# Performance work log

Measured on AMD Instinct MI355X. Metric: run time of the kernel, lower is better.

Reference implementation:

```python
import jax, jax.numpy as jnp
import numpy as np

DN = ('NCHW', 'OIHW', 'NCHW')

def _conv(x, w, padding):
    return jax.lax.conv_general_dilated(
        x, w, window_strides=(1, 1), padding=padding,
        dimension_numbers=DN)

def setup_inputs() -> dict:
    key = jax.random.key(0)
    k1, k2, k3, k4, k5 = jax.random.split(key, 5)
    nf = 40
    x = jax.random.normal(k1, (16, nf, 256, 256), dtype=jnp.float32)
    # PyTorch conv default init scale ~ 1/sqrt(fan_in)
    w2 = jax.random.normal(k2, (nf, nf, 1, 1), dtype=jnp.float32) / np.sqrt(nf)
    b2 = jax.random.normal(k3, (nf,), dtype=jnp.float32) * 0.01
    w3 = jax.random.normal(k4, (nf, nf, 3, 3), dtype=jnp.float32) / np.sqrt(nf * 9)
    w4 = jax.random.normal(k5, (nf, nf, 3, 3), dtype=jnp.float32) / np.sqrt(nf * 9)
    return {"x": x, "w2": w2, "b2": b2, "w3": w3, "w4": w4}

def reference(x, w2, b2, w3, w4):
    # k2: 1x1 conv + bias, then sigmoid gate (pixel attention)
    y = _conv(x, w2, padding='VALID') + b2[None, :, None, None]
    y = jax.nn.sigmoid(y)
    # k3: 3x3 conv (pad 1, no bias), gated elementwise
    out = _conv(x, w3, padding=((1, 1), (1, 1))) * y
    # k4: 3x3 conv (pad 1, no bias)
    out = _conv(out, w4, padding=((1, 1), (1, 1)))
    return out
```

## Files before the change

kernel.cpp:

```cpp
#include <hip/hip_runtime.h>
#include <hip/hip_bf16.h>

typedef __bf16 bf16;
typedef __bf16 bf16x2 __attribute__((ext_vector_type(2)));
typedef __bf16 bf16x4 __attribute__((ext_vector_type(4)));
typedef __bf16 bf16x8 __attribute__((ext_vector_type(8)));
typedef float f32x4 __attribute__((ext_vector_type(4)));

#define NF 40
#define HW 256
#define KPAD 384
#define MPAD 48

#define ZROW_ELEM_OFF (2 * MPAD * KPAD + MPAD * 64)
#define GATED_ELEM_OFF 40960
#define IMG_ELEMS ((size_t)16 * HW * HW * NF)
#define XT_ELEM_OFF (GATED_ELEM_OFF + IMG_ELEMS)
#define WS_FULL  ((GATED_ELEM_OFF + 2 * IMG_ELEMS) * 2)

#define PLANE ((size_t)HW * HW * 8)
#define IMGSTR ((size_t)HW * HW * NF)

#define RW 34
#define RU 612
#define GS 4896
#define NUNITS 3060
#define XS_ELEMS 24576

__device__ __forceinline__ void gload_lds16(const bf16* g, bf16* l) {
  __builtin_amdgcn_global_load_lds(
      (const __attribute__((address_space(1))) void*)g,
      (__attribute__((address_space(3))) void*)l, 16, 0, 0);
}

__global__ void prep_weights(const float* __restrict__ w2,
                             const float* __restrict__ w3,
                             const float* __restrict__ w4,
                             bf16* __restrict__ ws) {
  int i = blockIdx.x * 256 + threadIdx.x;
  const int T = MPAD * KPAD;
  if (i < T) {
    int co = i / KPAD, k = i % KPAD;
    float v3 = 0.f, v4 = 0.f;
    if (co < NF && k < 360) {
      int tap = k / NF, ci = k - tap * NF;
      int ky = tap / 3, kx = tap - ky * 3;
      int idx = ((co * NF + ci) * 3 + ky) * 3 + kx;
      v3 = w3[idx];
      v4 = w4[idx];
    }
    ws[i] = (bf16)v3;
    ws[T + i] = (bf16)v4;
  }
  if (i < MPAD * 64) {
    int co = i / 64, ci = i - co * 64;
    float v = 0.f;
    if (co < NF && ci < NF) v = w2[co * NF + ci];
    ws[2 * T + i] = (bf16)v;
  }
  if (i < 1024) ws[ZROW_ELEM_OFF + i] = (bf16)0.f;
}

__global__ __launch_bounds__(256, 8)
void transpose_nhwc(const float* __restrict__ x, bf16* __restrict__ xT) {
  __shared__ bf16 xs[5 * 2056];
  const int tid = threadIdx.x;
  const int row = blockIdx.x;
  const int n   = blockIdx.y;
  const size_t nb = (size_t)n * NF * HW * HW + (size_t)row * HW;

#pragma unroll
  for (int cc = 0; cc < 10; ++cc) {
    bf16x4 v;
#pragma unroll
    for (int j = 0; j < 4; ++j)
      v[j] = (bf16)x[nb + (size_t)(cc * 4 + j) * HW * HW + tid];
    *(bf16x4*)&xs[(cc >> 1) * 2056 + tid * 8 + (cc & 1) * 4] = v;
  }
  __syncthreads();

  const size_t ob = ((size_t)n * HW * HW + (size_t)row * HW) * NF;
#pragma unroll
  for (int k = 0; k < 10; ++k) {
    int u = tid + k * 256;
    int px = u / 10, c4 = u - px * 10;
    bf16x4 v = *(const bf16x4*)&xs[(c4 >> 1) * 2056 + px * 8 + (c4 & 1) * 4];
    *(bf16x4*)&xT[ob + (size_t)u * 4] = v;
  }
}

__global__ __launch_bounds__(512, 4)
void k1_gate(const bf16* __restrict__ xT, const float* __restrict__ b2,
             const bf16* __restrict__ ws, bf16* __restrict__ gated) {
  __shared__ bf16 xs[XS_ELEMS];

  const int tid  = threadIdx.x;
  const int lane = tid & 63;
  const int wid  = tid >> 6;
  const int l15  = lane & 15;
  const int lk   = lane >> 4;
  const int n    = blockIdx.z;
  const int X0   = blockIdx.x * 32;
  const int Y0   = blockIdx.y * 16;

  const bf16* W3A  = ws;
  const bf16* W2A  = ws + 2 * MPAD * KPAD;
  const bf16* zrow = ws + ZROW_ELEM_OFF;

  const bf16* bn = xT + (size_t)n * IMGSTR;
#pragma unroll
  for (int it = 0; it < 6; ++it) {
    int u0 = it * 512 + wid * 64;
    int u  = u0 + lane;
    int c   = u / RU;
    int rem = u - c * RU;
    int r   = rem / RW;
    int p   = rem - r * RW;
    int gy  = Y0 - 1 + r, gx = X0 - 1 + p;
    bool ok = (u < NUNITS) && ((unsigned)gy < HW) && ((unsigned)gx < HW);
    const bf16* src = ok ? (bn + (size_t)(gy * HW + gx) * NF + (c << 3)) : zrow;
    gload_lds16(src, &xs[u0 * 8]);
  }

  int gp3[12];
#pragma unroll
  for (int kk = 0; kk < 12; ++kk) {
    int k0 = kk * 32 + lk * 8;
    int kc = (k0 < 360) ? k0 : 0;
    int tap = kc / NF, ci0 = kc - tap * NF;
    int ky = tap / 3, kx = tap - ky * 3;
    gp3[kk] = (ci0 >> 3) * GS + (ky * RW + kx) * 8;
  }
  int gctr[2];
#pragma unroll
  for (int kk = 0; kk < 2; ++kk) {
    int k0 = kk * 32 + lk * 8;
    int ci0 = (k0 < NF) ? k0 : 0;
    gctr[kk] = (ci0 >> 3) * GS + (RW + 1) * 8;
  }
  int pb[4];
#pragma unroll
  for (int g = 0; g < 4; ++g) {
    int prow = wid * 2 + (g >> 1);
    int pcol = (g & 1) * 16 + l15;
    pb[g] = (prow * RW + pcol) * 8;
  }
  float b2v[3][4];
#pragma unroll
  for (int mt = 0; mt < 3; ++mt)
#pragma unroll
    for (int r = 0; r < 4; ++r) {
      int co = mt * 16 + lk * 4 + r;
      b2v[mt][r] = (co < NF) ? b2[co] : 0.f;
    }
  bf16x8 a2[2][3];
#pragma unroll
  for (int kk = 0; kk < 2; ++kk)
#pragma unroll
    for (int mt = 0; mt < 3; ++mt)
      a2[kk][mt] = *(const bf16x8*)&W2A[(mt * 16 + l15) * 64 + kk * 32 + lk * 8];

  __syncthreads();

  bf16x4 gv[4][3];
  {
    f32x4 g[4][3];
#pragma unroll
    for (int q = 0; q < 4; ++q)
#pragma unroll
      for (int mt = 0; mt < 3; ++mt) g[q][mt] = f32x4{0, 0, 0, 0};
#pragma unroll
    for (int kk = 0; kk < 2; ++kk)
#pragma unroll
      for (int q = 0; q < 4; ++q) {
        bf16x8 b = *(const bf16x8*)&xs[gctr[kk] + pb[q]];
#pragma unroll
        for (int mt = 0; mt < 3; ++mt)
          g[q][mt] = __builtin_amdgcn_mfma_f32_16x16x32_bf16(a2[kk][mt], b, g[q][mt], 0, 0, 0);
      }
#pragma unroll
    for (int q = 0; q < 4; ++q)
#pragma unroll
      for (int mt = 0; mt < 3; ++mt)
#pragma unroll
        for (int r = 0; r < 4; ++r)
          gv[q][mt][r] = (bf16)(1.f / (1.f + __expf(-(g[q][mt][r] + b2v[mt][r]))));
  }

  f32x4 f[4][3];
#pragma unroll
  for (int q = 0; q < 4; ++q)
#pragma unroll
    for (int mt = 0; mt < 3; ++mt) f[q][mt] = f32x4{0, 0, 0, 0};

#pragma unroll
  for (int kk = 0; kk < 12; ++kk) {
    bf16x8 a[3];
#pragma unroll
    for (int mt = 0; mt < 3; ++mt)
      a[mt] = *(const bf16x8*)&W3A[(mt * 16 + l15) * KPAD + kk * 32 + lk * 8];
#pragma unroll
    for (int q = 0; q < 4; ++q) {
      bf16x8 b = *(const bf16x8*)&xs[gp3[kk] + pb[q]];
#pragma unroll
      for (int mt = 0; mt < 3; ++mt)
        f[q][mt] = __builtin_amdgcn_mfma_f32_16x16x32_bf16(a[mt], b, f[q][mt], 0, 0, 0);
    }
  }

#pragma unroll
  for (int q = 0; q < 4; ++q) {
    int prow = wid * 2 + (q >> 1);
    int pcol = (q & 1) * 16 + l15;
    size_t pix8 = ((size_t)(Y0 + prow) * HW + (X0 + pcol)) * 8;
#pragma unroll
    for (int mt = 0; mt < 3; ++mt) {
      int co0 = mt * 16 + lk * 4;
      if (co0 < NF) {
        int cg = co0 >> 3;
        bf16x4 ov;
#pragma unroll
        for (int r = 0; r < 4; ++r)
          ov[r] = (bf16)(f[q][mt][r] * (float)gv[q][mt][r]);
        *(bf16x4*)&gated[(size_t)n * IMGSTR + (size_t)cg * PLANE + pix8 + (co0 & 7)] = ov;
      }
    }
  }
}

__global__ __launch_bounds__(512, 4)
void k2_conv(const bf16* __restrict__ gated, const bf16* __restrict__ ws,
             float* __restrict__ out) {
  __shared__ bf16 xs[XS_ELEMS];

  const int tid  = threadIdx.x;
  const int lane = tid & 63;
  const int wid  = tid >> 6;
  const int l15  = lane & 15;
  const int lk   = lane >> 4;
  const int n    = blockIdx.z;
  const int X0   = blockIdx.x * 32;
  const int Y0   = blockIdx.y * 16;

  const bf16* W4A  = ws + MPAD * KPAD;
  const bf16* zrow = ws + ZROW_ELEM_OFF;

  const bf16* bn = gated + (size_t)n * IMGSTR;
#pragma unroll
  for (int it = 0; it < 6; ++it) {
    int u0 = it * 512 + wid * 64;
    int u  = u0 + lane;
    int c   = u / RU;
    int rem = u - c * RU;
    int r   = rem / RW;
    int p   = rem - r * RW;
    int gy  = Y0 - 1 + r, gx = X0 - 1 + p;
    bool ok = (u < NUNITS) && ((unsigned)gy < HW) && ((unsigned)gx < HW);
    const bf16* src = ok ? (bn + (size_t)c * PLANE + (size_t)(gy * HW + gx) * 8) : zrow;
    gload_lds16(src, &xs[u0 * 8]);
  }

  int gp4[12];
#pragma unroll
  for (int kk = 0; kk < 12; ++kk) {
    int k0 = kk * 32 + lk * 8;
    int kc = (k0 < 360) ? k0 : 0;
    int tap = kc / NF, ci0 = kc - tap * NF;
    int ky = tap / 3, kx = tap - ky * 3;
    gp4[kk] = (ci0 >> 3) * GS + (ky * RW + kx) * 8;
  }
  int pb[4];
#pragma unroll
  for (int g = 0; g < 4; ++g) {
    int prow = wid * 2 + (g >> 1);
    int pcol = (g & 1) * 16 + l15;
    pb[g] = (prow * RW + pcol) * 8;
  }

  __syncthreads();

  f32x4 f[4][3];
#pragma unroll
  for (int q = 0; q < 4; ++q)
#pragma unroll
    for (int mt = 0; mt < 3; ++mt) f[q][mt] = f32x4{0, 0, 0, 0};

#pragma unroll
  for (int kk = 0; kk < 12; ++kk) {
    bf16x8 a[3];
#pragma unroll
    for (int mt = 0; mt < 3; ++mt)
      a[mt] = *(const bf16x8*)&W4A[(mt * 16 + l15) * KPAD + kk * 32 + lk * 8];
#pragma unroll
    for (int q = 0; q < 4; ++q) {
      bf16x8 b = *(const bf16x8*)&xs[gp4[kk] + pb[q]];
#pragma unroll
      for (int mt = 0; mt < 3; ++mt)
        f[q][mt] = __builtin_amdgcn_mfma_f32_16x16x32_bf16(a[mt], b, f[q][mt], 0, 0, 0);
    }
  }

  float* on = out + (size_t)n * NF * HW * HW;
#pragma unroll
  for (int q = 0; q < 4; ++q) {
    int prow = wid * 2 + (q >> 1);
    int pcol = (q & 1) * 16 + l15;
    float* orow = on + (size_t)(Y0 + prow) * HW + (X0 + pcol);
#pragma unroll
    for (int mt = 0; mt < 3; ++mt)
#pragma unroll
      for (int r = 0; r < 4; ++r) {
        int co = mt * 16 + lk * 4 + r;
        if (co < NF)
          orow[(size_t)co * HW * HW] = f[q][mt][r];
      }
  }
}

#define K1_RW 18
__global__ __launch_bounds__(512, 6)
void k1_gate_nchw(const float* __restrict__ x, const float* __restrict__ b2,
                  const bf16* __restrict__ ws, bf16* __restrict__ gated) {
  __shared__ bf16 xs[K1_RW * K1_RW * NF];

  const int tid  = threadIdx.x;
  const int lane = tid & 63;
  const int wid  = tid >> 6;
  const int l15  = lane & 15;
  const int lk   = lane >> 4;
  const int n    = blockIdx.z;
  const int X0   = blockIdx.x * 16;
  const int Y0   = blockIdx.y * 16;

  const bf16* W3A = ws;
  const bf16* W2A = ws + 2 * MPAD * KPAD;

  const float* xn = x + (size_t)n * NF * HW * HW;
  for (int i = tid; i < K1_RW * K1_RW * NF / 2; i += 512) {
    int cih = i / (K1_RW * K1_RW);
    int rem = i - cih * (K1_RW * K1_RW);
    int ci  = cih * 2;
    int yy  = rem / K1_RW, xx = rem - yy * K1_RW;
    int gy  = Y0 - 1 + yy, gx = X0 - 1 + xx;
    float v0 = 0.f, v1 = 0.f;
    if ((unsigned)gy < HW && (unsigned)gx < HW) {
      const float* p = xn + (size_t)ci * HW * HW + gy * HW + gx;
      v0 = p[0];
      v1 = p[HW * HW];
    }
    bf16x2 pr; pr[0] = (bf16)v0; pr[1] = (bf16)v1;
    *(bf16x2*)&xs[rem * NF + ci] = pr;
  }

  int off3[12];
#pragma unroll
  for (int kk = 0; kk < 12; ++kk) {
    int k0 = kk * 32 + lk * 8;
    int kc = (k0 < 360) ? k0 : 0;
    int tap = kc / NF, ci0 = kc - tap * NF;
    int ky = tap / 3, kx = tap - ky * 3;
    off3[kk] = (ky * K1_RW + kx) * NF + ci0;
  }
  int pb[2];
#pragma unroll
  for (int t2 = 0; t2 < 2; ++t2) {
    int pix = (wid * 2 + t2) * 16 + l15;
    int py = pix >> 4, px = pix & 15;
    pb[t2] = (py * K1_RW + px) * NF;
  }
  float b2v[3][4];
#pragma unroll
  for (int mt = 0; mt < 3; ++mt)
#pragma unroll
    for (int r = 0; r < 4; ++r) {
      int co = mt * 16 + lk * 4 + r;
      b2v[mt][r] = (co < NF) ? b2[co] : 0.f;
    }

  __syncthreads();

  bf16x4 gv[2][3];
  {
    f32x4 g[2][3];
#pragma unroll
    for (int t2 = 0; t2 < 2; ++t2)
#pragma unroll
      for (int mt = 0; mt < 3; ++mt) g[t2][mt] = f32x4{0, 0, 0, 0};
#pragma unroll
    for (int kk = 0; kk < 2; ++kk) {
      int k0 = kk * 32 + lk * 8;
      int goff = (K1_RW + 1) * NF + ((k0 < NF) ? k0 : 0);
      bf16x8 a[3];
#pragma unroll
      for (int mt = 0; mt < 3; ++mt)
        a[mt] = *(const bf16x8*)&W2A[(mt * 16 + l15) * 64 + k0];
#pragma unroll
      for (int t2 = 0; t2 < 2; ++t2) {
        bf16x8 b = *(const bf16x8*)&xs[pb[t2] + goff];
#pragma unroll
        for (int mt = 0; mt < 3; ++mt)
          g[t2][mt] = __builtin_amdgcn_mfma_f32_16x16x32_bf16(a[mt], b, g[t2][mt], 0, 0, 0);
      }
    }
#pragma unroll
    for (int t2 = 0; t2 < 2; ++t2)
#pragma unroll
      for (int mt = 0; mt < 3; ++mt)
#pragma unroll
        for (int r = 0; r < 4; ++r)
          gv[t2][mt][r] = (bf16)(1.f / (1.f + __expf(-(g[t2][mt][r] + b2v[mt][r]))));
  }

  f32x4 facc[2][3];
#pragma unroll
  for (int t2 = 0; t2 < 2; ++t2)
#pragma unroll
    for (int mt = 0; mt < 3; ++mt) facc[t2][mt] = f32x4{0, 0, 0, 0};

#pragma unroll
  for (int kk = 0; kk < 12; ++kk) {
    bf16x8 a[3];
#pragma unroll
    for (int mt = 0; mt < 3; ++mt)
      a[mt] = *(const bf16x8*)&W3A[(mt * 16 + l15) * KPAD + kk * 32 + lk * 8];
#pragma unroll
    for (int t2 = 0; t2 < 2; ++t2) {
      bf16x8 b = *(const bf16x8*)&xs[pb[t2] + off3[kk]];
#pragma unroll
      for (int mt = 0; mt < 3; ++mt)
        facc[t2][mt] = __builtin_amdgcn_mfma_f32_16x16x32_bf16(a[mt], b, facc[t2][mt], 0, 0, 0);
    }
  }

#pragma unroll
  for (int t2 = 0; t2 < 2; ++t2) {
    int pix = (wid * 2 + t2) * 16 + l15;
    int py = pix >> 4, px = pix & 15;
    size_t pix8 = ((size_t)(Y0 + py) * HW + (X0 + px)) * 8;
#pragma unroll
    for (int mt = 0; mt < 3; ++mt) {
      int co0 = mt * 16 + lk * 4;
      if (co0 < NF) {
        int cg = co0 >> 3;
        bf16x4 ov;
#pragma unroll
        for (int r = 0; r < 4; ++r)
          ov[r] = (bf16)(facc[t2][mt][r] * (float)gv[t2][mt][r]);
        *(bf16x4*)&gated[(size_t)n * IMGSTR + (size_t)cg * PLANE + pix8 + (co0 & 7)] = ov;
      }
    }
  }
}

extern "C" void kernel_launch(void* const* d_in, const int* in_sizes, int n_in,
                              void* d_out, int out_size, void* d_ws, size_t ws_size,
                              hipStream_t stream) {
  const float* x  = (const float*)d_in[0];
  const float* w2 = (const float*)d_in[1];
  const float* b2 = (const float*)d_in[2];
  const float* w3 = (const float*)d_in[3];
  const float* w4 = (const float*)d_in[4];
  float* out = (float*)d_out;
  bf16* ws   = (bf16*)d_ws;

  hipLaunchKernelGGL(prep_weights, dim3(72), dim3(256), 0, stream, w2, w3, w4, ws);

  bf16* gated = ws + GATED_ELEM_OFF;
  if (ws_size >= WS_FULL) {
    bf16* xT = ws + XT_ELEM_OFF;
    hipLaunchKernelGGL(transpose_nhwc, dim3(256, 16), dim3(256), 0, stream, x, xT);
    hipLaunchKernelGGL(k1_gate, dim3(8, 16, 16), dim3(512), 0, stream,
                       xT, b2, ws, gated);
  } else {
    hipLaunchKernelGGL(k1_gate_nchw, dim3(16, 16, 16), dim3(512), 0, stream,
                       x, b2, ws, gated);
  }
  hipLaunchKernelGGL(k2_conv, dim3(8, 16, 16), dim3(512), 0, stream,
                     gated, ws, out);
}
```

Baseline: 311.0 us.

## Sweep row strips per block with double-buffered async LDS halo loads

Both conv kernels now have each 256-thread block walk eight 8-row strips of a 64-row column band. The next strip's halo is prefetched into a second LDS buffer with global_load_lds while MFMAs run on the current one. This cuts block count, reuses per-thread index setup across strips, and overlaps global loads with compute. In exchange, each strip reloads the 2 halo rows, the grid shrinks to 512 blocks with fewer waves per block, and a barrier is added per strip.

```diff
diff --git a/kernel.cpp b/kernel.cpp
--- a/kernel.cpp
+++ b/kernel.cpp
@@ -21,11 +21,12 @@
 #define PLANE ((size_t)HW * HW * 8)
 #define IMGSTR ((size_t)HW * HW * NF)
 
-#define RW 34
-#define RU 612
-#define GS 4896
-#define NUNITS 3060
-#define XS_ELEMS 24576
+#define SRW 34
+#define SRH 10
+#define SRU 340
+#define SGS 2720
+#define SNU 1700
+#define SBUF 14336
 
 __device__ __forceinline__ void gload_lds16(const bf16* g, bf16* l) {
   __builtin_amdgcn_global_load_lds(
@@ -89,10 +90,10 @@
   }
 }
 
-__global__ __launch_bounds__(512, 4)
-void k1_gate(const bf16* __restrict__ xT, const float* __restrict__ b2,
-             const bf16* __restrict__ ws, bf16* __restrict__ gated) {
-  __shared__ bf16 xs[XS_ELEMS];
+__global__ __launch_bounds__(256, 2)
+void k1_sweep(const bf16* __restrict__ xT, const float* __restrict__ b2,
+              const bf16* __restrict__ ws, bf16* __restrict__ gated) {
+  __shared__ bf16 xs[2][SBUF];
 
   const int tid  = threadIdx.x;
   const int lane = tid & 63;
@@ -101,26 +102,12 @@
   const int lk   = lane >> 4;
   const int n    = blockIdx.z;
   const int X0   = blockIdx.x * 32;
-  const int Y0   = blockIdx.y * 16;
+  const int Yb   = blockIdx.y * 64;
 
   const bf16* W3A  = ws;
   const bf16* W2A  = ws + 2 * MPAD * KPAD;
   const bf16* zrow = ws + ZROW_ELEM_OFF;
-
-  const bf16* bn = xT + (size_t)n * IMGSTR;
-#pragma unroll
-  for (int it = 0; it < 6; ++it) {
-    int u0 = it * 512 + wid * 64;
-    int u  = u0 + lane;
-    int c   = u / RU;
-    int rem = u - c * RU;
-    int r   = rem / RW;
-    int p   = rem - r * RW;
-    int gy  = Y0 - 1 + r, gx = X0 - 1 + p;
-    bool ok = (u < NUNITS) && ((unsigned)gy < HW) && ((unsigned)gx < HW);
-    const bf16* src = ok ? (bn + (size_t)(gy * HW + gx) * NF + (c << 3)) : zrow;
-    gload_lds16(src, &xs[u0 * 8]);
-  }
+  const bf16* bn   = xT + (size_t)n * IMGSTR;
 
   int gp3[12];
 #pragma unroll
@@ -129,21 +116,21 @@
     int kc = (k0 < 360) ? k0 : 0;
     int tap = kc / NF, ci0 = kc - tap * NF;
     int ky = tap / 3, kx = tap - ky * 3;
-    gp3[kk] = (ci0 >> 3) * GS + (ky * RW + kx) * 8;
+    gp3[kk] = (ci0 >> 3) * SGS + (ky * SRW + kx) * 8;
   }
   int gctr[2];
 #pragma unroll
   for (int kk = 0; kk < 2; ++kk) {
     int k0 = kk * 32 + lk * 8;
     int ci0 = (k0 < NF) ? k0 : 0;
-    gctr[kk] = (ci0 >> 3) * GS + (RW + 1) * 8;
+    gctr[kk] = (ci0 >> 3) * SGS + (SRW + 1) * 8;
   }
   int pb[4];
 #pragma unroll
-  for (int g = 0; g < 4; ++g) {
-    int prow = wid * 2 + (g >> 1);
-    int pcol = (g & 1) * 16 + l15;
-    pb[g] = (prow * RW + pcol) * 8;
+  for (int q = 0; q < 4; ++q) {
+    int prow = wid * 2 + (q >> 1);
+    int pcol = (q & 1) * 16 + l15;
+    pb[q] = (prow * SRW + pcol) * 8;
   }
   float b2v[3][4];
 #pragma unroll
@@ -160,78 +147,124 @@
     for (int mt = 0; mt < 3; ++mt)
       a2[kk][mt] = *(const bf16x8*)&W2A[(mt * 16 + l15) * 64 + kk * 32 + lk * 8];
 
+  int uc8[7], ur[7], ugx[7], uld[7];
+  bool uok[7];
+#pragma unroll
+  for (int it = 0; it < 7; ++it) {
+    int u0 = it * 256 + wid * 64;
+    int u  = u0 + lane;
+    int c   = u / SRU;
+    int rem = u - c * SRU;
+    int r   = rem / SRW;
+    int p   = rem - r * SRW;
+    int gx  = X0 - 1 + p;
+    uok[it] = (u < SNU) && ((unsigned)gx < HW);
+    uc8[it] = (c << 3);
+    ur[it]  = r;
+    ugx[it] = ((unsigned)gx < HW) ? gx : 0;
+    uld[it] = u0 * 8;
+  }
+
+  {
+    int ys = Yb - 1;
+#pragma unroll
+    for (int it = 0; it < 7; ++it) {
+      int gy = ys + ur[it];
+      bool ok = uok[it] && ((unsigned)gy < HW);
+      const bf16* src = ok ? (bn + (size_t)(gy * HW + ugx[it]) * NF + uc8[it]) : zrow;
+      gload_lds16(src, &xs[0][uld[it]]);
+    }
+  }
   __syncthreads();
 
-  bf16x4 gv[4][3];
-  {
-    f32x4 g[4][3];
+  for (int s = 0; s < 8; ++s) {
+    const bf16* buf = xs[s & 1];
+
+    if (s < 7) {
+      int ys = Yb + (s + 1) * 8 - 1;
+      bf16* nbuf = xs[(s & 1) ^ 1];
+#pragma unroll
+      for (int it = 0; it < 7; ++it) {
+        int gy = ys + ur[it];
+        bool ok = uok[it] && ((unsigned)gy < HW);
+        const bf16* src = ok ? (bn + (size_t)(gy * HW + ugx[it]) * NF + uc8[it]) : zrow;
+        gload_lds16(src, &nbuf[uld[it]]);
+      }
+    }
+
+    bf16x4 gv[4][3];
+    {
+      f32x4 g[4][3];
+#pragma unroll
+      for (int q = 0; q < 4; ++q)
+#pragma unroll
+        for (int mt = 0; mt < 3; ++mt) g[q][mt] = f32x4{0, 0, 0, 0};
+#pragma unroll
+      for (int kk = 0; kk < 2; ++kk)
+#pragma unroll
+        for (int q = 0; q < 4; ++q) {
+          bf16x8 b = *(const bf16x8*)&buf[gctr[kk] + pb[q]];
+#pragma unroll
+          for (int mt = 0; mt < 3; ++mt)
+            g[q][mt] = __builtin_amdgcn_mfma_f32_16x16x32_bf16(a2[kk][mt], b, g[q][mt], 0, 0, 0);
+        }
+#pragma unroll
+      for (int q = 0; q < 4; ++q)
+#pragma unroll
+        for (int mt = 0; mt < 3; ++mt)
+#pragma unroll
+          for (int r = 0; r < 4; ++r)
+            gv[q][mt][r] = (bf16)(1.f / (1.f + __expf(-(g[q][mt][r] + b2v[mt][r]))));
+    }
+
+    f32x4 f[4][3];
 #pragma unroll
     for (int q = 0; q < 4; ++q)
 #pragma unroll
-      for (int mt = 0; mt < 3; ++mt) g[q][mt] = f32x4{0, 0, 0, 0};
-#pragma unroll
-    for (int kk = 0; kk < 2; ++kk)
+      for (int mt = 0; mt < 3; ++mt) f[q][mt] = f32x4{0, 0, 0, 0};
+
+#pragma unroll
+    for (int kk = 0; kk < 12; ++kk) {
+      bf16x8 a[3];
+#pragma unroll
+      for (int mt = 0; mt < 3; ++mt)
+        a[mt] = *(const bf16x8*)&W3A[(mt * 16 + l15) * KPAD + kk * 32 + lk * 8];
 #pragma unroll
       for (int q = 0; q < 4; ++q) {
-        bf16x8 b = *(const bf16x8*)&xs[gctr[kk] + pb[q]];
+        bf16x8 b = *(const bf16x8*)&buf[gp3[kk] + pb[q]];
 #pragma unroll
         for (int mt = 0; mt < 3; ++mt)
-          g[q][mt] = __builtin_amdgcn_mfma_f32_16x16x32_bf16(a2[kk][mt], b, g[q][mt], 0, 0, 0);
-      }
-#pragma unroll
-    for (int q = 0; q < 4; ++q)
-#pragma unroll
-      for (int mt = 0; mt < 3; ++mt)
-#pragma unroll
-        for (int r = 0; r < 4; ++r)
-          gv[q][mt][r] = (bf16)(1.f / (1.f + __expf(-(g[q][mt][r] + b2v[mt][r]))));
-  }
-
-  f32x4 f[4][3];
-#pragma unroll
-  for (int q = 0; q < 4; ++q)
-#pragma unroll
-    for (int mt = 0; mt < 3; ++mt) f[q][mt] = f32x4{0, 0, 0, 0};
-
-#pragma unroll
-  for (int kk = 0; kk < 12; ++kk) {
-    bf16x8 a[3];
-#pragma unroll
-    for (int mt = 0; mt < 3; ++mt)
-      a[mt] = *(const bf16x8*)&W3A[(mt * 16 + l15) * KPAD + kk * 32 + lk * 8];
+          f[q][mt] = __builtin_amdgcn_mfma_f32_16x16x32_bf16(a[mt], b, f[q][mt], 0, 0, 0);
+      }
+    }
+
 #pragma unroll
     for (int q = 0; q < 4; ++q) {
-      bf16x8 b = *(const bf16x8*)&xs[gp3[kk] + pb[q]];
-#pragma unroll
-      for (int mt = 0; mt < 3; ++mt)
-        f[q][mt] = __builtin_amdgcn_mfma_f32_16x16x32_bf16(a[mt], b, f[q][mt], 0, 0, 0);
-    }
-  }
-
-#pragma unroll
-  for (int q = 0; q < 4; ++q) {
-    int prow = wid * 2 + (q >> 1);
-    int pcol = (q & 1) * 16 + l15;
-    size_t pix8 = ((size_t)(Y0 + prow) * HW + (X0 + pcol)) * 8;
-#pragma unroll
-    for (int mt = 0; mt < 3; ++mt) {
-      int co0 = mt * 16 + lk * 4;
-      if (co0 < NF) {
-        int cg = co0 >> 3;
-        bf16x4 ov;
-#pragma unroll
-        for (int r = 0; r < 4; ++r)
-          ov[r] = (bf16)(f[q][mt][r] * (float)gv[q][mt][r]);
-        *(bf16x4*)&gated[(size_t)n * IMGSTR + (size_t)cg * PLANE + pix8 + (co0 & 7)] = ov;
-      }
-    }
-  }
-}
-
-__global__ __launch_bounds__(512, 4)
-void k2_conv(const bf16* __restrict__ gated, const bf16* __restrict__ ws,
-             float* __restrict__ out) {
-  __shared__ bf16 xs[XS_ELEMS];
+      int prow = wid * 2 + (q >> 1);
+      int pcol = (q & 1) * 16 + l15;
+      size_t pix8 = ((size_t)(Yb + s * 8 + prow) * HW + (X0 + pcol)) * 8;
+#pragma unroll
+      for (int mt = 0; mt < 3; ++mt) {
+        int co0 = mt * 16 + lk * 4;
+        if (co0 < NF) {
+          int cg = co0 >> 3;
+          bf16x4 ov;
+#pragma unroll
+          for (int r = 0; r < 4; ++r)
+            ov[r] = (bf16)(f[q][mt][r] * (float)gv[q][mt][r]);
+          *(bf16x4*)&gated[(size_t)n * IMGSTR + (size_t)cg * PLANE + pix8 + (co0 & 7)] = ov;
+        }
+      }
+    }
+
+    __syncthreads();
+  }
+}
+
+__global__ __launch_bounds__(256, 2)
+void k2_sweep(const bf16* __restrict__ gated, const bf16* __restrict__ ws,
+              float* __restrict__ out) {
+  __shared__ bf16 xs[2][SBUF];
 
   const int tid  = threadIdx.x;
   const int lane = tid & 63;
@@ -240,25 +273,11 @@
   const int lk   = lane >> 4;
   const int n    = blockIdx.z;
   const int X0   = blockIdx.x * 32;
-  const int Y0   = blockIdx.y * 16;
+  const int Yb   = blockIdx.y * 64;
 
   const bf16* W4A  = ws + MPAD * KPAD;
   const bf16* zrow = ws + ZROW_ELEM_OFF;
-
-  const bf16* bn = gated + (size_t)n * IMGSTR;
-#pragma unroll
-  for (int it = 0; it < 6; ++it) {
-    int u0 = it * 512 + wid * 64;
-    int u  = u0 + lane;
-    int c   = u / RU;
-    int rem = u - c * RU;
-    int r   = rem / RW;
-    int p   = rem - r * RW;
-    int gy  = Y0 - 1 + r, gx = X0 - 1 + p;
-    bool ok = (u < NUNITS) && ((unsigned)gy < HW) && ((unsigned)gx < HW);
-    const bf16* src = ok ? (bn + (size_t)c * PLANE + (size_t)(gy * HW + gx) * 8) : zrow;
-    gload_lds16(src, &xs[u0 * 8]);
-  }
+  const bf16* bn   = gated + (size_t)n * IMGSTR;
 
   int gp4[12];
 #pragma unroll
@@ -267,53 +286,100 @@
     int kc = (k0 < 360) ? k0 : 0;
     int tap = kc / NF, ci0 = kc - tap * NF;
     int ky = tap / 3, kx = tap - ky * 3;
-    gp4[kk] = (ci0 >> 3) * GS + (ky * RW + kx) * 8;
+    gp4[kk] = (ci0 >> 3) * SGS + (ky * SRW + kx) * 8;
   }
   int pb[4];
-#pragma unroll
-  for (int g = 0; g < 4; ++g) {
-    int prow = wid * 2 + (g >> 1);
-    int pcol = (g & 1) * 16 + l15;
-    pb[g] = (prow * RW + pcol) * 8;
-  }
-
-  __syncthreads();
-
-  f32x4 f[4][3];
-#pragma unroll
-  for (int q = 0; q < 4; ++q)
-#pragma unroll
-    for (int mt = 0; mt < 3; ++mt) f[q][mt] = f32x4{0, 0, 0, 0};
-
-#pragma unroll
-  for (int kk = 0; kk < 12; ++kk) {
-    bf16x8 a[3];
-#pragma unroll
-    for (int mt = 0; mt < 3; ++mt)
-      a[mt] = *(const bf16x8*)&W4A[(mt * 16 + l15) * KPAD + kk * 32 + lk * 8];
-#pragma unroll
-    for (int q = 0; q < 4; ++q) {
-      bf16x8 b = *(const bf16x8*)&xs[gp4[kk] + pb[q]];
-#pragma unroll
-      for (int mt = 0; mt < 3; ++mt)
-        f[q][mt] = __builtin_amdgcn_mfma_f32_16x16x32_bf16(a[mt], b, f[q][mt], 0, 0, 0);
-    }
-  }
-
-  float* on = out + (size_t)n * NF * HW * HW;
 #pragma unroll
   for (int q = 0; q < 4; ++q) {
     int prow = wid * 2 + (q >> 1);
     int pcol = (q & 1) * 16 + l15;
-    float* orow = on + (size_t)(Y0 + prow) * HW + (X0 + pcol);
-#pragma unroll
-    for (int mt = 0; mt < 3; ++mt)
-#pragma unroll
-      for (int r = 0; r < 4; ++r) {
-        int co = mt * 16 + lk * 4 + r;
-        if (co < NF)
-          orow[(size_t)co * HW * HW] = f[q][mt][r];
-      }
+    pb[q] = (prow * SRW + pcol) * 8;
+  }
+
+  int ucp[7], ur[7], ugx[7], uld[7];
+  bool uok[7];
+#pragma unroll
+  for (int it = 0; it < 7; ++it) {
+    int u0 = it * 256 + wid * 64;
+    int u  = u0 + lane;
+    int c   = u / SRU;
+    int rem = u - c * SRU;
+    int r   = rem / SRW;
+    int p   = rem - r * SRW;
+    int gx  = X0 - 1 + p;
+    uok[it] = (u < SNU) && ((unsigned)gx < HW);
+    ucp[it] = (c < 5) ? c : 0;
+    ur[it]  = r;
+    ugx[it] = ((unsigned)gx < HW) ? gx : 0;
+    uld[it] = u0 * 8;
+  }
+
+  {
+    int ys = Yb - 1;
+#pragma unroll
+    for (int it = 0; it < 7; ++it) {
+      int gy = ys + ur[it];
+      bool ok = uok[it] && ((unsigned)gy < HW);
+      const bf16* src = ok ? (bn + (size_t)ucp[it] * PLANE + (size_t)(gy * HW + ugx[it]) * 8) : zrow;
+      gload_lds16(src, &xs[0][uld[it]]);
+    }
+  }
+  __syncthreads();
+
+  float* on = out + (size_t)n * NF * HW * HW;
+
+  for (int s = 0; s < 8; ++s) {
+    const bf16* buf = xs[s & 1];
+
+    if (s < 7) {
+      int ys = Yb + (s + 1) * 8 - 1;
+      bf16* nbuf = xs[(s & 1) ^ 1];
+#pragma unroll
+      for (int it = 0; it < 7; ++it) {
+        int gy = ys + ur[it];
+        bool ok = uok[it] && ((unsigned)gy < HW);
+        const bf16* src = ok ? (bn + (size_t)ucp[it] * PLANE + (size_t)(gy * HW + ugx[it]) * 8) : zrow;
+        gload_lds16(src, &nbuf[uld[it]]);
+      }
+    }
+
+    f32x4 f[4][3];
+#pragma unroll
+    for (int q = 0; q < 4; ++q)
+#pragma unroll
+      for (int mt = 0; mt < 3; ++mt) f[q][mt] = f32x4{0, 0, 0, 0};
+
+#pragma unroll
+    for (int kk = 0; kk < 12; ++kk) {
+      bf16x8 a[3];
+#pragma unroll
+      for (int mt = 0; mt < 3; ++mt)
+        a[mt] = *(const bf16x8*)&W4A[(mt * 16 + l15) * KPAD + kk * 32 + lk * 8];
+#pragma unroll
+      for (int q = 0; q < 4; ++q) {
+        bf16x8 b = *(const bf16x8*)&buf[gp4[kk] + pb[q]];
+#pragma unroll
+        for (int mt = 0; mt < 3; ++mt)
+          f[q][mt] = __builtin_amdgcn_mfma_f32_16x16x32_bf16(a[mt], b, f[q][mt], 0, 0, 0);
+      }
+    }
+
+#pragma unroll
+    for (int q = 0; q < 4; ++q) {
+      int prow = wid * 2 + (q >> 1);
+      int pcol = (q & 1) * 16 + l15;
+      float* orow = on + (size_t)(Yb + s * 8 + prow) * HW + (X0 + pcol);
+#pragma unroll
+      for (int mt = 0; mt < 3; ++mt)
+#pragma unroll
+        for (int r = 0; r < 4; ++r) {
+          int co = mt * 16 + lk * 4 + r;
+          if (co < NF)
+            orow[(size_t)co * HW * HW] = f[q][mt][r];
+        }
+    }
+
+    __syncthreads();
   }
 }
 
@@ -469,12 +535,12 @@
   if (ws_size >= WS_FULL) {
     bf16* xT = ws + XT_ELEM_OFF;
     hipLaunchKernelGGL(transpose_nhwc, dim3(256, 16), dim3(256), 0, stream, x, xT);
-    hipLaunchKernelGGL(k1_gate, dim3(8, 16, 16), dim3(512), 0, stream,
+    hipLaunchKernelGGL(k1_sweep, dim3(8, 4, 16), dim3(256), 0, stream,
                        xT, b2, ws, gated);
   } else {
     hipLaunchKernelGGL(k1_gate_nchw, dim3(16, 16, 16), dim3(512), 0, stream,
                        x, b2, ws, gated);
   }
-  hipLaunchKernelGGL(k2_conv, dim3(8, 16, 16), dim3(512), 0, stream,
+  hipLaunchKernelGGL(k2_sweep, dim3(8, 4, 16), dim3(256), 0, stream,
                      gated, ws, out);
 }
```

Result: faster. 285.4 us (-8.2%).
